# Performance work log

Hardware: AMD Instinct MI355X
Metric: run time of the kernel (lower is better)

The kernel has to match this reference:

```python
import jax, jax.numpy as jnp
import numpy as np

T, B, I, H = 2048, 64, 256, 256

def setup_inputs() -> dict:
    key = jax.random.key(0)
    k_x, k_wih, k_whh = jax.random.split(key, 3)
    x = jax.random.normal(k_x, (T, B, I), dtype=jnp.float32)
    h0 = jnp.zeros((1, B, H), dtype=jnp.float32)
    # nn.RNN weight_ih_l0 init: U(-1/sqrt(H), 1/sqrt(H)); shape [H, I]
    bound = 1.0 / np.sqrt(H)
    W_ih = jax.random.uniform(k_wih, (H, I), minval=-bound, maxval=bound, dtype=jnp.float32)
    # IndRNN recurrent weight: diagonal vector, U(-1, 1); biases are zeroed.
    w_hh = jax.random.uniform(k_whh, (H,), minval=-1.0, maxval=1.0, dtype=jnp.float32)
    return {"x": x, "h0": h0, "W_ih": W_ih, "w_hh": w_hh}

def reference(x, h0, W_ih, w_hh):
    # Precompute the input projection for all timesteps (the only GEMM):
    # [T, B, H] = x @ W_ih^T  (biases are zero)
    xW = jnp.einsum('tbi,hi->tbh', x, W_ih)

    def step(h, xw_t):
        # IndRNN: diagonal recurrence -> elementwise multiply instead of matmul
        h_new = jax.nn.relu(xw_t + h * w_hh)
        return h_new, h_new

    h_last, outputs = jax.lax.scan(step, h0[0], xW)
    return outputs, h_last[None]  # ([T,B,H], [1,B,H]) matching nn.RNN
```

## Files before the change

kernel.cpp:

```cpp
#include <hip/hip_runtime.h>

typedef short v8s __attribute__((ext_vector_type(8)));
typedef float v4f __attribute__((ext_vector_type(4)));

#define BH 16384
#define TBH 33554432
#define SCAN_TILE 128
#define NTILE 16

__device__ __forceinline__ ushort f2bf(float f) {
  uint u = __float_as_uint(f);
  u += 0x7FFF + ((u >> 16) & 1);
  return (ushort)(u >> 16);
}

__global__ __launch_bounds__(512) void indrnn_gemm(
    const float* __restrict__ A,
    const float* __restrict__ W,
    ushort* __restrict__ C)
{
  __shared__ ushort As[128 * 72];
  __shared__ ushort Bs[256 * 72];

  const int tid  = threadIdx.x;
  const int lane = tid & 63;
  const int wid  = tid >> 6;
  const int wm   = wid >> 2;
  const int wn   = wid & 3;
  const int m0   = blockIdx.x * 128;

  const int l15 = lane & 15;
  const int lhi = lane >> 4;

  v4f acc[4][4] = {};

  for (int kc = 0; kc < 4; ++kc) {
    #pragma unroll
    for (int j = 0; j < 4; ++j) {
      int f    = j * 512 + tid;
      int row  = f >> 4;
      int colf = f & 15;
      const float4 a4 = *(const float4*)(A + ((size_t)(m0 + row) << 8) + kc * 64 + colf * 4);
      ushort4 b4 = make_ushort4(f2bf(a4.x), f2bf(a4.y), f2bf(a4.z), f2bf(a4.w));
      *(ushort4*)(As + row * 72 + colf * 4) = b4;
    }
    #pragma unroll
    for (int j = 0; j < 8; ++j) {
      int f    = j * 512 + tid;
      int row  = f >> 4;
      int colf = f & 15;
      const float4 a4 = *(const float4*)(W + ((size_t)row << 8) + kc * 64 + colf * 4);
      ushort4 b4 = make_ushort4(f2bf(a4.x), f2bf(a4.y), f2bf(a4.z), f2bf(a4.w));
      *(ushort4*)(Bs + row * 72 + colf * 4) = b4;
    }
    __syncthreads();

    #pragma unroll
    for (int kk = 0; kk < 2; ++kk) {
      const int koff = kk * 32 + lhi * 8;
      v8s af[4], bf[4];
      #pragma unroll
      for (int mt = 0; mt < 4; ++mt)
        af[mt] = *(const v8s*)(As + (wm * 64 + mt * 16 + l15) * 72 + koff);
      #pragma unroll
      for (int nt = 0; nt < 4; ++nt)
        bf[nt] = *(const v8s*)(Bs + (wn * 64 + nt * 16 + l15) * 72 + koff);
      #pragma unroll
      for (int mt = 0; mt < 4; ++mt)
        #pragma unroll
        for (int nt = 0; nt < 4; ++nt)
          acc[mt][nt] = __builtin_amdgcn_mfma_f32_16x16x32_bf16(af[mt], bf[nt], acc[mt][nt], 0, 0, 0);
    }
    __syncthreads();
  }

  #pragma unroll
  for (int mt = 0; mt < 4; ++mt) {
    #pragma unroll
    for (int nt = 0; nt < 4; ++nt) {
      #pragma unroll
      for (int r = 0; r < 4; ++r) {
        int row = m0 + wm * 64 + mt * 16 + lhi * 4 + r;
        int col = wn * 64 + nt * 16 + l15;
        C[((size_t)row << 8) + col] = f2bf(acc[mt][nt][r]);
      }
    }
  }
}

__global__ __launch_bounds__(128) void indrnn_scan(
    const ushort* __restrict__ xw,
    const float* __restrict__ h0,
    const float* __restrict__ w_hh,
    float* __restrict__ out)
{
  __shared__ __align__(16) ushort tile[3][SCAN_TILE * 64];

  const int lane = threadIdx.x & 63;
  const int wv   = threadIdx.x >> 6;
  const int ch0  = blockIdx.x * 64;
  const int ch   = ch0 + lane;

  const size_t psrc0 = (size_t)(lane >> 3) * BH + (size_t)ch0 + ((lane & 7) << 3);

  auto stage = [&](int ti) {
    const ushort* src = xw + (size_t)ti * SCAN_TILE * BH + psrc0;
    ushort* dst = &tile[ti % 3][0];
    #pragma unroll
    for (int j = 0; j < 16; ++j) {
      __builtin_amdgcn_global_load_lds(
          (const float*)(src + (size_t)j * 8 * BH),
          (float*)(dst + j * 512), 16, 0, 0);
    }
  };

  float h = 0.0f, w = 0.0f;
  if (wv == 0) {
    h = h0[ch];
    w = w_hh[ch & 255];
  } else {
    stage(0);
    stage(1);
    asm volatile("s_waitcnt vmcnt(16)" ::: "memory");
  }
  asm volatile("" ::: "memory");
  __builtin_amdgcn_s_barrier();
  __builtin_amdgcn_sched_barrier(0);

  for (int i = 0; i < NTILE; ++i) {
    if (wv == 0) {
      const ushort* tp = &tile[i % 3][lane];
      float* po = out + (size_t)i * SCAN_TILE * BH + ch;
      #pragma unroll
      for (int t = 0; t < SCAN_TILE; t += 16) {
        ushort v[16];
        #pragma unroll
        for (int j = 0; j < 16; ++j) v[j] = tp[(t + j) * 64];
        #pragma unroll
        for (int j = 0; j < 16; ++j) {
          float xv = __uint_as_float((uint)v[j] << 16);
          h = fmaxf(fmaf(h, w, xv), 0.0f);
          po[(size_t)(t + j) * BH] = h;
        }
      }
    } else {
      if (i + 2 < NTILE) {
        stage(i + 2);
        asm volatile("s_waitcnt vmcnt(16)" ::: "memory");
      } else {
        asm volatile("s_waitcnt vmcnt(0)" ::: "memory");
      }
    }
    asm volatile("" ::: "memory");
    __builtin_amdgcn_s_barrier();
    __builtin_amdgcn_sched_barrier(0);
  }

  if (wv == 0) out[(size_t)TBH + ch] = h;
}

extern "C" void kernel_launch(void* const* d_in, const int* in_sizes, int n_in,
                              void* d_out, int out_size, void* d_ws, size_t ws_size,
                              hipStream_t stream) {
  const float* x    = (const float*)d_in[0];
  const float* h0   = (const float*)d_in[1];
  const float* W_ih = (const float*)d_in[2];
  const float* w_hh = (const float*)d_in[3];
  float* out = (float*)d_out;
  ushort* xw = (ushort*)d_ws;

  indrnn_gemm<<<dim3(1024), dim3(512), 0, stream>>>(x, W_ih, xw);
  indrnn_scan<<<dim3(256), dim3(128), 0, stream>>>(xw, h0, w_hh, out);
}
```

Measured before the change: 298.6 us.

## Parallelize IndRNN scan over time segments with clamped-affine composition

Replaces the sequential per-channel scan with a three-phase segmented scan. Time is split into 16 segments, and each segment is summarized as a clamped affine map (product, offset, lower and upper clamp). A fix-up kernel then composes the prefix maps and recomputes the outputs for its segment. This exposes 4x more parallel blocks, aimed at the latency-bound serial recurrence. The cost is a second read of xw and an extra launch, and the change only takes effect if the workspace is large enough; otherwise it falls back to the old kernel.

```diff
diff --git a/kernel.cpp b/kernel.cpp
--- a/kernel.cpp
+++ b/kernel.cpp
@@ -5,6 +5,8 @@
 
 #define BH 16384
 #define TBH 33554432
+#define SEG 16
+#define SEGT 128
 #define SCAN_TILE 128
 #define NTILE 16
 
@@ -86,6 +88,92 @@
       }
     }
   }
+}
+
+__global__ __launch_bounds__(256) void indrnn_seg(
+    const ushort* __restrict__ xw,
+    const float* __restrict__ w_hh,
+    float4* __restrict__ fn)
+{
+  const int chgrp = blockIdx.x & 63;
+  const int seg   = blockIdx.x >> 6;
+  const int ch    = chgrp * 256 + threadIdx.x;
+  const float w   = w_hh[ch & 255];
+  const ushort* px = xw + (size_t)seg * SEGT * BH + ch;
+
+  float p = 1.0f, a = 0.0f, lo = -3.402823466e38f, hi = 3.402823466e38f;
+
+  uint b0[16], b1[16];
+  auto ldb = [&](uint (&buf)[16], int kb) {
+    const ushort* q = px + (size_t)kb * 16 * BH;
+    #pragma unroll
+    for (int j = 0; j < 16; ++j) buf[j] = q[(size_t)j * BH];
+  };
+  auto comp = [&](uint (&buf)[16]) {
+    #pragma unroll
+    for (int j = 0; j < 16; ++j) {
+      float xv = __uint_as_float(buf[j] << 16);
+      float A = fmaf(w, lo, xv);
+      float B = fmaf(w, hi, xv);
+      lo = fmaxf(0.0f, fminf(A, B));
+      hi = fmaxf(0.0f, fmaxf(A, B));
+      a  = fmaf(w, a, xv);
+      p *= w;
+    }
+  };
+
+  ldb(b0, 0); ldb(b1, 1);
+  for (int kb = 0; kb < 8; kb += 2) {
+    comp(b0); if (kb + 2 < 8) ldb(b0, kb + 2);
+    comp(b1); if (kb + 3 < 8) ldb(b1, kb + 3);
+  }
+  fn[(size_t)seg * BH + ch] = make_float4(p, a, lo, hi);
+}
+
+__global__ __launch_bounds__(256) void indrnn_fix(
+    const ushort* __restrict__ xw,
+    const float* __restrict__ h0,
+    const float* __restrict__ w_hh,
+    const float4* __restrict__ fn,
+    float* __restrict__ out)
+{
+  const int chgrp = blockIdx.x & 63;
+  const int seg   = blockIdx.x >> 6;
+  const int ch    = chgrp * 256 + threadIdx.x;
+  const float w   = w_hh[ch & 255];
+
+  float h = h0[ch];
+  for (int s = 0; s < seg; ++s) {
+    const float4 F = fn[(size_t)s * BH + ch];
+    h = fminf(fmaxf(fmaf(F.x, h, F.y), F.z), F.w);
+  }
+
+  const ushort* px = xw + (size_t)seg * SEGT * BH + ch;
+  float*        po = out + (size_t)seg * SEGT * BH + ch;
+
+  uint b0[16], b1[16];
+  auto ldb = [&](uint (&buf)[16], int kb) {
+    const ushort* q = px + (size_t)kb * 16 * BH;
+    #pragma unroll
+    for (int j = 0; j < 16; ++j) buf[j] = q[(size_t)j * BH];
+  };
+  auto cp = [&](uint (&buf)[16], int kb) {
+    float* o = po + (size_t)kb * 16 * BH;
+    #pragma unroll
+    for (int j = 0; j < 16; ++j) {
+      float xv = __uint_as_float(buf[j] << 16);
+      h = fmaxf(fmaf(h, w, xv), 0.0f);
+      o[(size_t)j * BH] = h;
+    }
+  };
+
+  ldb(b0, 0); ldb(b1, 1);
+  for (int kb = 0; kb < 8; kb += 2) {
+    cp(b0, kb);     if (kb + 2 < 8) ldb(b0, kb + 2);
+    cp(b1, kb + 1); if (kb + 3 < 8) ldb(b1, kb + 3);
+  }
+
+  if (seg == SEG - 1) out[(size_t)TBH + ch] = h;
 }
 
 __global__ __launch_bounds__(128) void indrnn_scan(
@@ -170,5 +258,13 @@
   ushort* xw = (ushort*)d_ws;
 
   indrnn_gemm<<<dim3(1024), dim3(512), 0, stream>>>(x, W_ih, xw);
-  indrnn_scan<<<dim3(256), dim3(128), 0, stream>>>(xw, h0, w_hh, out);
-}
+
+  const size_t need = (64ull << 20) + (size_t)SEG * BH * sizeof(float4);
+  if (ws_size >= need) {
+    float4* fn = (float4*)((char*)d_ws + (64ull << 20));
+    indrnn_seg<<<dim3(1024), dim3(256), 0, stream>>>(xw, w_hh, fn);
+    indrnn_fix<<<dim3(1024), dim3(256), 0, stream>>>(xw, h0, w_hh, fn, out);
+  } else {
+    indrnn_scan<<<dim3(256), dim3(128), 0, stream>>>(xw, h0, w_hh, out);
+  }
+}
```

After: 286.1 us. 4.2% less time.
